# Optimization experiments

Measured on AMD Instinct MI355X. Metric: run time of the kernel, lower is better.

## Reference

```python
import jax, jax.numpy as jnp
import numpy as np

T, DIM, HID = 8192, 1024, 4096

def setup_inputs() -> dict:
    key = jax.random.key(0)
    k1, k2, k3 = jax.random.split(key, 3)
    x = jax.random.normal(k1, (T, DIM), dtype=jnp.float32)
    # torch Linear weight layout: [out_features, in_features]
    W_fc = jax.random.normal(k2, (HID, DIM), dtype=jnp.float32) * 0.02
    W_proj = jax.random.normal(k3, (DIM, HID), dtype=jnp.float32) * 0.02
    return {"x": x, "W_fc": W_fc, "W_proj": W_proj}

def reference(x, W_fc, W_proj):
    # fc: x @ W_fc^T  -> relu -> square -> proj: @ W_proj^T
    h = jnp.einsum('td,hd->th', x, W_fc)      # [T, HID]
    h = jnp.square(jax.nn.relu(h))            # relu(h)^2 (relu^2 activation)
    return jnp.einsum('th,dh->td', h, W_proj) # [T, DIM]
```

## Files before the change

### kernel.cpp

```cpp
#include <hip/hip_runtime.h>
#include <stdint.h>


typedef __attribute__((ext_vector_type(8))) short bf16x8;
typedef __attribute__((ext_vector_type(4))) float f32x4;

typedef const __attribute__((address_space(1))) unsigned int* gas_u32p;
typedef __attribute__((address_space(3))) unsigned int* las_u32p;

__device__ __forceinline__ void load16_to_lds(const void* gptr, void* lptr) {
    __builtin_amdgcn_global_load_lds((gas_u32p)gptr, (las_u32p)lptr, 16, 0, 0);
}

__device__ __forceinline__ void dsr128(bf16x8& d, unsigned off) {
    asm volatile("ds_read_b128 %0, %1" : "=v"(d) : "v"(off));
}

__device__ __forceinline__ unsigned short f2bf(float f) {
    unsigned int u = __float_as_uint(f);
    u += 0x7FFFu + ((u >> 16) & 1u);
    return (unsigned short)(u >> 16);
}

#define LGKM(n) do { \
    asm volatile("s_waitcnt lgkmcnt(%0)" :: "i"(n) : "memory"); \
    __builtin_amdgcn_sched_barrier(0); } while (0)
#define VMC(n) do { \
    asm volatile("s_waitcnt vmcnt(%0)" :: "i"(n) : "memory"); \
    __builtin_amdgcn_sched_barrier(0); } while (0)

__global__ void cvt_all(const float4* __restrict__ x,  ushort4* __restrict__ xb,
                        const float4* __restrict__ wf, ushort4* __restrict__ wfb,
                        const float4* __restrict__ wp, ushort4* __restrict__ wpb)
{
    const int base = blockIdx.x * 1024 + threadIdx.x;
    #pragma unroll
    for (int j = 0; j < 4; j++) {
        const int i = base + j * 256;
        const float4* s; ushort4* d; int k;
        if (i < (1 << 21))            { s = x;  d = xb;  k = i; }
        else if (i < 3 * (1 << 20))   { s = wf; d = wfb; k = i - (1 << 21); }
        else                          { s = wp; d = wpb; k = i - 3 * (1 << 20); }
        float4 v = s[k];
        ushort4 o;
        o.x = f2bf(v.x); o.y = f2bf(v.y); o.z = f2bf(v.z); o.w = f2bf(v.w);
        d[k] = o;
    }
}

__global__ __launch_bounds__(512, 2)
void gemm_skew1(const unsigned short* __restrict__ A,
                const unsigned short* __restrict__ B,
                unsigned short* __restrict__ C, int M, int N, int K)
{
    constexpr int AKH  = 16384;
    constexpr int BKH  = 16384;
    constexpr int BOFF = 2 * AKH;
    constexpr int BUFB = 2 * AKH + 2 * BKH;
    (void)M;

    __shared__ char lds[2 * BUFB];

    const int tid  = threadIdx.x;
    const int lane = tid & 63;
    const int wave = tid >> 6;
    const int wm   = wave >> 2;
    const int wn   = wave & 3;
    const int quad = lane >> 4;
    const int m16  = lane & 15;

    const int gx = gridDim.x;
    int flat = blockIdx.y * gx + blockIdx.x;
    const int cpx = (gx * gridDim.y) >> 3;
    flat = (flat & 7) * cpx + (flat >> 3);
    const long bm0 = (long)(flat / gx) * 256;
    const long bn0 = (long)(flat % gx) * 256;

    const int srow   = tid >> 2;
    const int schunk = (tid & 3) ^ ((tid >> 3) & 3);
    const unsigned short* gA = A + (bm0 + srow) * (long)K + schunk * 8;
    const unsigned short* gB = B + (bn0 + srow) * (long)K + schunk * 8;

    unsigned offA[8], offB[4];
    #pragma unroll
    for (int i = 0; i < 8; i++) {
        const unsigned lo = (unsigned)((wm * 128 + i * 16 + m16) * 64 + quad * 16);
        offA[i] = lo ^ (((lo >> 7) & 3) << 4);
    }
    #pragma unroll
    for (int j = 0; j < 4; j++) {
        const unsigned lo = (unsigned)((wn * 64 + j * 16 + m16) * 64 + quad * 16);
        offB[j] = lo ^ (((lo >> 7) & 3) << 4);
    }

    const unsigned ldsbase =
        (unsigned)(unsigned long long)(las_u32p)(void*)lds;

    f32x4 acc[8][4];
    #pragma unroll
    for (int i = 0; i < 8; i++)
        #pragma unroll
        for (int j = 0; j < 4; j++)
            acc[i][j] = (f32x4)0.0f;

    const int NT = K >> 6;

    #define STG1(t, kh) do { \
        char* _dA = (char*)lds + ((t) & 1) * BUFB + (kh) * AKH + tid * 16; \
        const unsigned short* _sA = gA + (long)(t) * 64 + (kh) * 32; \
        load16_to_lds(_sA, _dA); \
        load16_to_lds(_sA + 128l * K, _dA + 8192); \
        char* _dB = (char*)lds + ((t) & 1) * BUFB + BOFF + (kh) * BKH + tid * 16; \
        const unsigned short* _sB = gB + (long)(t) * 64 + (kh) * 32; \
        load16_to_lds(_sB, _dB); \
        load16_to_lds(_sB + 128l * K, _dB + 8192); } while (0)

    STG1(0, 0); STG1(0, 1);
    if (NT > 1) {
        STG1(1, 0);
        VMC(4);
    } else {
        VMC(0);
    }
    __builtin_amdgcn_s_barrier();

    for (int t = 0; t < NT; ++t) {
        const unsigned bufo = ldsbase + (unsigned)((t & 1) * BUFB);
        bf16x8 a0[4], b0[4], a0b[4], a1[4], b1[4], a1b[4];

        #pragma unroll
        for (int i = 0; i < 4; i++) dsr128(a0[i],  bufo + offA[i]);
        #pragma unroll
        for (int j = 0; j < 4; j++) dsr128(b0[j],  bufo + BOFF + offB[j]);
        #pragma unroll
        for (int i = 0; i < 4; i++) dsr128(a0b[i], bufo + offA[4 + i]);
        if (t + 1 < NT) STG1(t + 1, 1);
        __builtin_amdgcn_s_barrier();

        LGKM(4);
        __builtin_amdgcn_s_setprio(1);
        #pragma unroll
        for (int i = 0; i < 4; i++)
            #pragma unroll
            for (int j = 0; j < 4; j++)
                acc[i][j] = __builtin_amdgcn_mfma_f32_16x16x32_bf16(
                    a0[i], b0[j], acc[i][j], 0, 0, 0);
        __builtin_amdgcn_s_setprio(0);

        #pragma unroll
        for (int i = 0; i < 4; i++) dsr128(a1[i],  bufo + AKH + offA[i]);
        #pragma unroll
        for (int j = 0; j < 4; j++) dsr128(b1[j],  bufo + BOFF + BKH + offB[j]);
        #pragma unroll
        for (int i = 0; i < 4; i++) dsr128(a1b[i], bufo + AKH + offA[4 + i]);

        LGKM(12);
        __builtin_amdgcn_s_setprio(1);
        #pragma unroll
        for (int i = 0; i < 4; i++)
            #pragma unroll
            for (int j = 0; j < 4; j++)
                acc[4 + i][j] = __builtin_amdgcn_mfma_f32_16x16x32_bf16(
                    a0b[i], b0[j], acc[4 + i][j], 0, 0, 0);
        __builtin_amdgcn_s_setprio(0);
        __builtin_amdgcn_s_barrier();

        if (t + 2 < NT) STG1(t + 2, 0);

        LGKM(4);
        __builtin_amdgcn_s_setprio(1);
        #pragma unroll
        for (int i = 0; i < 4; i++)
            #pragma unroll
            for (int j = 0; j < 4; j++)
                acc[i][j] = __builtin_amdgcn_mfma_f32_16x16x32_bf16(
                    a1[i], b1[j], acc[i][j], 0, 0, 0);
        __builtin_amdgcn_s_setprio(0);

        LGKM(0);
        __builtin_amdgcn_s_setprio(1);
        #pragma unroll
        for (int i = 0; i < 4; i++)
            #pragma unroll
            for (int j = 0; j < 4; j++)
                acc[4 + i][j] = __builtin_amdgcn_mfma_f32_16x16x32_bf16(
                    a1b[i], b1[j], acc[4 + i][j], 0, 0, 0);
        __builtin_amdgcn_s_setprio(0);

        if (t + 2 < NT) VMC(4);
        else            VMC(0);
        __builtin_amdgcn_s_barrier();
    }
    #undef STG1

    const long baseRow = bm0 + wm * 128 + quad * 4;
    const long baseCol = bn0 + wn * 64 + m16;
    #pragma unroll
    for (int i = 0; i < 8; i++) {
        #pragma unroll
        for (int j = 0; j < 4; j++) {
            #pragma unroll
            for (int r = 0; r < 4; r++) {
                float v = acc[i][j][r];
                v = (v > 0.0f) ? v * v : 0.0f;
                const long row = baseRow + i * 16 + r;
                const long col = baseCol + j * 16;
                C[row * (long)N + col] = f2bf(v);
            }
        }
    }
}

__global__ __launch_bounds__(512, 2)
void gemm_skew(const unsigned short* __restrict__ A,
               const unsigned short* __restrict__ B,
               float* __restrict__ C, int M, int N, int K)
{
    constexpr int AKH  = 16384;
    constexpr int BKH  = 8192;
    constexpr int BOFF = 2 * AKH;
    constexpr int BUFB = 2 * AKH + 2 * BKH;
    (void)M;

    __shared__ char lds[2 * BUFB];

    const int tid  = threadIdx.x;
    const int lane = tid & 63;
    const int wave = tid >> 6;
    const int wm   = wave >> 1;
    const int wn   = wave & 1;
    const int quad = lane >> 4;
    const int m16  = lane & 15;

    const int gx = gridDim.x;
    int flat = blockIdx.y * gx + blockIdx.x;
    const int cpx = (gx * gridDim.y) >> 3;
    flat = (flat & 7) * cpx + (flat >> 3);
    const long bm0 = (long)(flat / gx) * 256;
    const long bn0 = (long)(flat % gx) * 128;

    const int srow   = tid >> 2;
    const int schunk = (tid & 3) ^ ((tid >> 3) & 3);
    const unsigned short* gA = A + (bm0 + srow) * (long)K + schunk * 8;
    const unsigned short* gB = B + (bn0 + srow) * (long)K + schunk * 8;

    unsigned offA[4], offB[4];
    #pragma unroll
    for (int i = 0; i < 4; i++) {
        const unsigned lo = (unsigned)((wm * 64 + i * 16 + m16) * 64 + quad * 16);
        offA[i] = lo ^ (((lo >> 7) & 3) << 4);
    }
    #pragma unroll
    for (int j = 0; j < 4; j++) {
        const unsigned lo = (unsigned)((wn * 64 + j * 16 + m16) * 64 + quad * 16);
        offB[j] = lo ^ (((lo >> 7) & 3) << 4);
    }

    const unsigned ldsbase =
        (unsigned)(unsigned long long)(las_u32p)(void*)lds;

    f32x4 acc[4][4];
    #pragma unroll
    for (int i = 0; i < 4; i++)
        #pragma unroll
        for (int j = 0; j < 4; j++)
            acc[i][j] = (f32x4)0.0f;

    const int NT = K >> 6;

    #define STAGE2(t, kh) do { \
        char* _dA = (char*)lds + ((t) & 1) * BUFB + (kh) * AKH + tid * 16; \
        const unsigned short* _sA = gA + (long)(t) * 64 + (kh) * 32; \
        load16_to_lds(_sA, _dA); \
        load16_to_lds(_sA + 128l * K, _dA + 8192); \
        char* _dB = (char*)lds + ((t) & 1) * BUFB + BOFF + (kh) * BKH + tid * 16; \
        load16_to_lds(gB + (long)(t) * 64 + (kh) * 32, _dB); } while (0)

    STAGE2(0, 0); STAGE2(0, 1);
    if (NT > 1) {
        STAGE2(1, 0);
        asm volatile("s_waitcnt vmcnt(3)" ::: "memory");
    } else {
        asm volatile("s_waitcnt vmcnt(0)" ::: "memory");
    }
    __builtin_amdgcn_sched_barrier(0);
    __builtin_amdgcn_s_barrier();

    for (int t = 0; t < NT; ++t) {
        const unsigned bufo = ldsbase + (unsigned)((t & 1) * BUFB);
        bf16x8 a0[4], b0[4], a1[4], b1[4];

        #pragma unroll
        for (int i = 0; i < 4; i++) dsr128(a0[i], bufo + offA[i]);
        #pragma unroll
        for (int j = 0; j < 4; j++) dsr128(b0[j], bufo + BOFF + offB[j]);
        #pragma unroll
        for (int i = 0; i < 4; i++) dsr128(a1[i], bufo + AKH + offA[i]);
        #pragma unroll
        for (int j = 0; j < 4; j++) dsr128(b1[j], bufo + BOFF + BKH + offB[j]);
        if (t + 1 < NT) STAGE2(t + 1, 1);
        __builtin_amdgcn_s_barrier();
        asm volatile("s_waitcnt lgkmcnt(8)" ::: "memory");
        __builtin_amdgcn_sched_barrier(0);
        __builtin_amdgcn_s_setprio(1);
        #pragma unroll
        for (int i = 0; i < 4; i++)
            #pragma unroll
            for (int j = 0; j < 4; j++)
                acc[i][j] = __builtin_amdgcn_mfma_f32_16x16x32_bf16(
                    a0[i], b0[j], acc[i][j], 0, 0, 0);
        __builtin_amdgcn_s_setprio(0);
        __builtin_amdgcn_s_barrier();

        if (t + 2 < NT) STAGE2(t + 2, 0);
        asm volatile("s_waitcnt lgkmcnt(0)" ::: "memory");
        __builtin_amdgcn_sched_barrier(0);
        __builtin_amdgcn_s_setprio(1);
        #pragma unroll
        for (int i = 0; i < 4; i++)
            #pragma unroll
            for (int j = 0; j < 4; j++)
                acc[i][j] = __builtin_amdgcn_mfma_f32_16x16x32_bf16(
                    a1[i], b1[j], acc[i][j], 0, 0, 0);
        __builtin_amdgcn_s_setprio(0);
        if (t + 2 < NT) asm volatile("s_waitcnt vmcnt(3)" ::: "memory");
        else            asm volatile("s_waitcnt vmcnt(0)" ::: "memory");
        __builtin_amdgcn_sched_barrier(0);
        __builtin_amdgcn_s_barrier();
    }
    #undef STAGE2

    const long baseRow = bm0 + wm * 64 + quad * 4;
    const long baseCol = bn0 + wn * 64 + m16;
    #pragma unroll
    for (int i = 0; i < 4; i++) {
        #pragma unroll
        for (int j = 0; j < 4; j++) {
            #pragma unroll
            for (int r = 0; r < 4; r++) {
                const long row = baseRow + i * 16 + r;
                const long col = baseCol + j * 16;
                C[row * (long)N + col] = acc[i][j][r];
            }
        }
    }
}

extern "C" void kernel_launch(void* const* d_in, const int* in_sizes, int n_in,
                              void* d_out, int out_size, void* d_ws, size_t ws_size,
                              hipStream_t stream) {
    (void)in_sizes; (void)n_in; (void)out_size; (void)ws_size;

    const int T = 8192, DIM = 1024, HID = 4096;

    const float* x     = (const float*)d_in[0];
    const float* W_fc  = (const float*)d_in[1];
    const float* W_prj = (const float*)d_in[2];
    float* out = (float*)d_out;

    char* ws = (char*)d_ws;
    unsigned short* h   = (unsigned short*)ws;
    unsigned short* xb  = (unsigned short*)(ws + (64l << 20));
    unsigned short* wfb = (unsigned short*)(ws + (80l << 20));
    unsigned short* wpb = (unsigned short*)(ws + (88l << 20));

    cvt_all<<<4096, 256, 0, stream>>>(
        (const float4*)x,     (ushort4*)xb,
        (const float4*)W_fc,  (ushort4*)wfb,
        (const float4*)W_prj, (ushort4*)wpb);

    gemm_skew1<<<dim3(HID / 256, T / 256), dim3(512), 0, stream>>>(
        xb, wfb, h, T, HID, DIM);

    gemm_skew<<<dim3(DIM / 128, T / 256), dim3(512), 0, stream>>>(
        h, wpb, out, T, DIM, HID);
}
```

Before: 241.0 us.

## Restructure fc GEMM into 1024-thread 256x512 tiles with triple-buffered K=32 stages

Replaces the fc GEMM kernel with a 16-wave, 1024-thread block that computes a 256x512 output tile. The K loop now steps by 32 instead of 64 and rotates through three LDS buffers, prefetching two stages ahead with a single barrier per iteration. The aim is more B reuse per block and fewer barriers and stalls in the main loop. In exchange it runs one block per CU with a larger LDS footprint, processes more, smaller K-steps, and the grid has half as many blocks.

```diff
diff --git a/kernel.cpp b/kernel.cpp
--- a/kernel.cpp
+++ b/kernel.cpp
@@ -48,24 +48,23 @@
     }
 }
 
-__global__ __launch_bounds__(512, 2)
-void gemm_skew1(const unsigned short* __restrict__ A,
-                const unsigned short* __restrict__ B,
-                unsigned short* __restrict__ C, int M, int N, int K)
+__global__ __launch_bounds__(1024, 1)
+void gemm_fc(const unsigned short* __restrict__ A,
+             const unsigned short* __restrict__ B,
+             unsigned short* __restrict__ C, int M, int N, int K)
 {
-    constexpr int AKH  = 16384;
-    constexpr int BKH  = 16384;
-    constexpr int BOFF = 2 * AKH;
-    constexpr int BUFB = 2 * AKH + 2 * BKH;
+    constexpr int AB   = 16384;
+    constexpr int BB   = 32768;
+    constexpr int BUFB = AB + BB;
     (void)M;
 
-    __shared__ char lds[2 * BUFB];
+    __shared__ char lds[3 * BUFB];
 
     const int tid  = threadIdx.x;
     const int lane = tid & 63;
     const int wave = tid >> 6;
-    const int wm   = wave >> 2;
-    const int wn   = wave & 3;
+    const int wm   = wave >> 3;
+    const int wn   = wave & 7;
     const int quad = lane >> 4;
     const int m16  = lane & 15;
 
@@ -74,7 +73,7 @@
     const int cpx = (gx * gridDim.y) >> 3;
     flat = (flat & 7) * cpx + (flat >> 3);
     const long bm0 = (long)(flat / gx) * 256;
-    const long bn0 = (long)(flat % gx) * 256;
+    const long bn0 = (long)(flat % gx) * 512;
 
     const int srow   = tid >> 2;
     const int schunk = (tid & 3) ^ ((tid >> 3) & 3);
@@ -90,10 +89,10 @@
     #pragma unroll
     for (int j = 0; j < 4; j++) {
         const unsigned lo = (unsigned)((wn * 64 + j * 16 + m16) * 64 + quad * 16);
-        offB[j] = lo ^ (((lo >> 7) & 3) << 4);
-    }
-
-    const unsigned ldsbase =
+        offB[j] = AB + (lo ^ (((lo >> 7) & 3) << 4));
+    }
+
+    const unsigned base =
         (unsigned)(unsigned long long)(las_u32p)(void*)lds;
 
     f32x4 acc[8][4];
@@ -103,39 +102,36 @@
         for (int j = 0; j < 4; j++)
             acc[i][j] = (f32x4)0.0f;
 
-    const int NT = K >> 6;
-
-    #define STG1(t, kh) do { \
-        char* _dA = (char*)lds + ((t) & 1) * BUFB + (kh) * AKH + tid * 16; \
-        const unsigned short* _sA = gA + (long)(t) * 64 + (kh) * 32; \
-        load16_to_lds(_sA, _dA); \
-        load16_to_lds(_sA + 128l * K, _dA + 8192); \
-        char* _dB = (char*)lds + ((t) & 1) * BUFB + BOFF + (kh) * BKH + tid * 16; \
-        const unsigned short* _sB = gB + (long)(t) * 64 + (kh) * 32; \
-        load16_to_lds(_sB, _dB); \
-        load16_to_lds(_sB + 128l * K, _dB + 8192); } while (0)
-
-    STG1(0, 0); STG1(0, 1);
+    const int NT = K >> 5;
+
+    #define STG(po_, t_) do { \
+        char* _d = (char*)lds + (po_) + tid * 16; \
+        const unsigned short* _sA = gA + (long)(t_) * 32; \
+        load16_to_lds(_sA, _d); \
+        const unsigned short* _sB = gB + (long)(t_) * 32; \
+        load16_to_lds(_sB, _d + AB); \
+        load16_to_lds(_sB + 256l * K, _d + AB + 16384); } while (0)
+
+    STG(0, 0);
     if (NT > 1) {
-        STG1(1, 0);
-        VMC(4);
+        STG(BUFB, 1);
+        VMC(3);
     } else {
         VMC(0);
     }
     __builtin_amdgcn_s_barrier();
 
+    unsigned co = 0, no = BUFB, po = 2 * BUFB;
+
     for (int t = 0; t < NT; ++t) {
-        const unsigned bufo = ldsbase + (unsigned)((t & 1) * BUFB);
-        bf16x8 a0[4], b0[4], a0b[4], a1[4], b1[4], a1b[4];
-
-        #pragma unroll
-        for (int i = 0; i < 4; i++) dsr128(a0[i],  bufo + offA[i]);
-        #pragma unroll
-        for (int j = 0; j < 4; j++) dsr128(b0[j],  bufo + BOFF + offB[j]);
-        #pragma unroll
-        for (int i = 0; i < 4; i++) dsr128(a0b[i], bufo + offA[4 + i]);
-        if (t + 1 < NT) STG1(t + 1, 1);
-        __builtin_amdgcn_s_barrier();
+        bf16x8 a[8], b[4];
+
+        #pragma unroll
+        for (int j = 0; j < 4; j++) dsr128(b[j], base + co + offB[j]);
+        #pragma unroll
+        for (int i = 0; i < 8; i++) dsr128(a[i], base + co + offA[i]);
+
+        if (t + 2 < NT) STG(po, t + 2);
 
         LGKM(4);
         __builtin_amdgcn_s_setprio(1);
@@ -144,54 +140,26 @@
             #pragma unroll
             for (int j = 0; j < 4; j++)
                 acc[i][j] = __builtin_amdgcn_mfma_f32_16x16x32_bf16(
-                    a0[i], b0[j], acc[i][j], 0, 0, 0);
+                    a[i], b[j], acc[i][j], 0, 0, 0);
         __builtin_amdgcn_s_setprio(0);
 
-        #pragma unroll
-        for (int i = 0; i < 4; i++) dsr128(a1[i],  bufo + AKH + offA[i]);
-        #pragma unroll
-        for (int j = 0; j < 4; j++) dsr128(b1[j],  bufo + BOFF + BKH + offB[j]);
-        #pragma unroll
-        for (int i = 0; i < 4; i++) dsr128(a1b[i], bufo + AKH + offA[4 + i]);
-
-        LGKM(12);
+        LGKM(0);
         __builtin_amdgcn_s_setprio(1);
         #pragma unroll
         for (int i = 0; i < 4; i++)
             #pragma unroll
             for (int j = 0; j < 4; j++)
                 acc[4 + i][j] = __builtin_amdgcn_mfma_f32_16x16x32_bf16(
-                    a0b[i], b0[j], acc[4 + i][j], 0, 0, 0);
+                    a[4 + i], b[j], acc[4 + i][j], 0, 0, 0);
         __builtin_amdgcn_s_setprio(0);
-        __builtin_amdgcn_s_barrier();
-
-        if (t + 2 < NT) STG1(t + 2, 0);
-
-        LGKM(4);
-        __builtin_amdgcn_s_setprio(1);
-        #pragma unroll
-        for (int i = 0; i < 4; i++)
-            #pragma unroll
-            for (int j = 0; j < 4; j++)
-                acc[i][j] = __builtin_amdgcn_mfma_f32_16x16x32_bf16(
-                    a1[i], b1[j], acc[i][j], 0, 0, 0);
-        __builtin_amdgcn_s_setprio(0);
-
-        LGKM(0);
-        __builtin_amdgcn_s_setprio(1);
-        #pragma unroll
-        for (int i = 0; i < 4; i++)
-            #pragma unroll
-            for (int j = 0; j < 4; j++)
-                acc[4 + i][j] = __builtin_amdgcn_mfma_f32_16x16x32_bf16(
-                    a1b[i], b1[j], acc[4 + i][j], 0, 0, 0);
-        __builtin_amdgcn_s_setprio(0);
-
-        if (t + 2 < NT) VMC(4);
+
+        if (t + 2 < NT) VMC(3);
         else            VMC(0);
         __builtin_amdgcn_s_barrier();
-    }
-    #undef STG1
+
+        const unsigned tmp = po; po = co; co = no; no = tmp;
+    }
+    #undef STG
 
     const long baseRow = bm0 + wm * 128 + quad * 4;
     const long baseCol = bn0 + wn * 64 + m16;
@@ -369,7 +337,7 @@
         (const float4*)W_fc,  (ushort4*)wfb,
         (const float4*)W_prj, (ushort4*)wpb);
 
-    gemm_skew1<<<dim3(HID / 256, T / 256), dim3(512), 0, stream>>>(
+    gemm_fc<<<dim3(HID / 512, T / 256), dim3(1024), 0, stream>>>(
         xb, wfb, h, T, HID, DIM);
 
     gemm_skew<<<dim3(DIM / 128, T / 256), dim3(512), 0, stream>>>(
```

After: 874.8 us. +263.0%, slower.
